# Kernel optimization log

Hardware: AMD Instinct MI355X
Metric: run time of the kernel (lower is better)

Reference implementation:

```python
import jax, jax.numpy as jnp
import numpy as np

N = 65536        # total nodes
E = 2097152      # total edges (avg degree 32)
B = 1024         # graphs / proteins
FXD = 78         # atom feature dim
DIM = 32         # GIN hidden dim
EMB = 128        # protein embedding dim
OUTD = 128       # output_dim
VOCAB = 26       # CHARPROTLEN + 1
PLEN = 1000      # protein sequence length (conv in_channels)
KS = 8           # conv kernel size
CLEN = EMB - KS + 1  # 121
NF = 32          # n_filters


def setup_inputs() -> dict:
    key = jax.random.key(0)
    ks = jax.random.split(key, 30)
    g = lambda k, s: (jax.random.normal(k, s, dtype=jnp.float32) * 0.05)
    inp = {
        "x": jax.random.normal(ks[0], (N, FXD), dtype=jnp.float32),
        "edge_index": jax.random.randint(ks[1], (2, E), 0, N, dtype=jnp.int32),
        "batch": jnp.sort(jax.random.randint(ks[2], (N,), 0, B, dtype=jnp.int32)),
        "target": jax.random.randint(ks[3], (B, PLEN), 0, VOCAB, dtype=jnp.int32),
        # GIN layer 1 MLP
        "w1a": g(ks[4], (FXD, DIM)), "b1a": jnp.zeros((DIM,), jnp.float32),
        "w1b": g(ks[5], (DIM, DIM)), "b1b": jnp.zeros((DIM,), jnp.float32),
        # GIN layers 2-5 MLPs (stacked)
        "wa": g(ks[6], (4, DIM, DIM)), "ba": jnp.zeros((4, DIM), jnp.float32),
        "wb": g(ks[7], (4, DIM, DIM)), "bb": jnp.zeros((4, DIM), jnp.float32),
        # BatchNorm affine params for bn1..bn5
        "gamma": jnp.ones((5, DIM), jnp.float32),
        "beta": jnp.zeros((5, DIM), jnp.float32),
        # drug head
        "w_fcxd": g(ks[8], (DIM, OUTD)), "b_fcxd": jnp.zeros((OUTD,), jnp.float32),
        # protein branch
        "emb": g(ks[9], (VOCAB, EMB)),
        "conv_w": g(ks[10], (NF, PLEN, KS)),  # OIH layout
        "conv_b": jnp.zeros((NF,), jnp.float32),
        "w_fcxt": g(ks[11], (NF * CLEN, OUTD)), "b_fcxt": jnp.zeros((OUTD,), jnp.float32),
        # joint head
        "w_fc1": g(ks[12], (256, 1024)), "b_fc1": jnp.zeros((1024,), jnp.float32),
        "w_fc2": g(ks[13], (1024, 256)), "b_fc2": jnp.zeros((256,), jnp.float32),
        "w_out": g(ks[14], (256, 1)), "b_out": jnp.zeros((1,), jnp.float32),
    }
    return inp


def reference(x, edge_index, batch, target,
              w1a, b1a, w1b, b1b, wa, ba, wb, bb, gamma, beta,
              w_fcxd, b_fcxd, emb, conv_w, conv_b, w_fcxt, b_fcxt,
              w_fc1, b_fc1, w_fc2, b_fc2, w_out, b_out):
    n_nodes = x.shape[0]
    n_graphs = target.shape[0]
    src, dst = edge_index[0], edge_index[1]

    def gin_bn(h, wi, bi, wo, bo, g, bt):
        # GINConv (eps=0): nn((1+eps)*x + sum_{j->i} x_j), then ReLU, then BatchNorm1d (batch stats)
        agg = jax.ops.segment_sum(h[src], dst, num_segments=n_nodes) + h
        h = jnp.maximum(agg @ wi + bi, 0.0) @ wo + bo
        h = jnp.maximum(h, 0.0)
        m = h.mean(axis=0)
        v = h.var(axis=0)  # biased, matches torch BN normalization
        return g * (h - m) * jax.lax.rsqrt(v + 1e-5) + bt

    h = gin_bn(x, w1a, b1a, w1b, b1b, gamma[0], beta[0])
    for i in range(4):
        h = gin_bn(h, wa[i], ba[i], wb[i], bb[i], gamma[i + 1], beta[i + 1])

    # global add pool over graphs
    hg = jax.ops.segment_sum(h, batch, num_segments=n_graphs)  # [B, 32]
    xd = jnp.maximum(hg @ w_fcxd + b_fcxd, 0.0)  # [B, 128] (dropout inactive in eval)

    # protein branch: embed then Conv1d over the embedding axis (in_channels = seq positions)
    e = emb[target]  # [B, 1000, 128]
    c = jax.lax.conv_general_dilated(e, conv_w, window_strides=(1,), padding="VALID",
                                     dimension_numbers=("NCH", "OIH", "NCH"))
    c = c + conv_b[None, :, None]  # [B, 32, 121]
    xt = c.reshape(n_graphs, NF * CLEN) @ w_fcxt + b_fcxt  # [B, 128], no activation in original

    xc = jnp.concatenate([xd, xt], axis=1)  # [B, 256]
    xc = jnp.maximum(xc @ w_fc1 + b_fc1, 0.0)
    xc = jnp.maximum(xc @ w_fc2 + b_fc2, 0.0)
    return xc @ w_out + b_out  # [B, 1]
```

## Files before the change

### kernel.cpp

```cpp
#include <hip/hip_runtime.h>
#include <hip/hip_fp16.h>

#define N_NODES 65536
#define N_EDGES 2097152
#define NB      1024
#define FXD     78
#define DIM     32
#define EMBD    128
#define OUTD    128
#define VOCAB   26
#define PLEN    1000
#define KS      8
#define CLEN    121
#define NF      32
#define FCX     (NF*CLEN)
#define NBKT    256
#define EPB     8192
#define NSLICE  256


__global__ __launch_bounds__(256) void k_bhist(
    const int* __restrict__ ei, int* __restrict__ bktCnt)
{
    __shared__ int h[NBKT];
    int tid = threadIdx.x;
    h[tid] = 0;
    __syncthreads();
    long base = (long)blockIdx.x * EPB;
    #pragma unroll 4
    for (int q=0; q<EPB/256; ++q) {
        int d = ei[N_EDGES + base + q*256 + tid];
        atomicAdd(&h[d>>8], 1);
    }
    __syncthreads();
    atomicAdd(&bktCnt[tid], h[tid]);
}

__global__ __launch_bounds__(256) void k_bscan(
    const int* __restrict__ bktCnt, int* __restrict__ bktBase, int* __restrict__ bktCur)
{
    __shared__ int s[NBKT];
    int t = threadIdx.x;
    int v = bktCnt[t];
    s[t] = v;
    __syncthreads();
    for (int off=1; off<256; off<<=1) {
        int tv = (t >= off) ? s[t-off] : 0;
        __syncthreads();
        s[t] += tv;
        __syncthreads();
    }
    int ex = s[t] - v;
    bktBase[t] = ex;
    bktCur[t] = ex;
    if (t == 255) bktBase[256] = s[255];
}

__global__ __launch_bounds__(256) void k_bucketA(
    const int* __restrict__ ei, int* __restrict__ bktCur, unsigned int* __restrict__ pairs)
{
    __shared__ unsigned int raw[EPB];
    __shared__ unsigned int srt[EPB];
    __shared__ unsigned char bOf[EPB];
    __shared__ int hist[NBKT], sc[NBKT], lcur[NBKT], gbase[NBKT];
    int tid = threadIdx.x;
    hist[tid] = 0;
    __syncthreads();
    int eb = blockIdx.x * EPB;
    for (int i=tid; i<EPB; i+=256) {
        int s = ei[eb+i];
        int d = ei[N_EDGES+eb+i];
        raw[i] = ((unsigned int)d<<16) | (unsigned int)s;
        atomicAdd(&hist[d>>8], 1);
    }
    __syncthreads();
    int v = hist[tid];
    sc[tid] = v;
    __syncthreads();
    for (int off=1; off<256; off<<=1) {
        int tv = (tid >= off) ? sc[tid-off] : 0;
        __syncthreads();
        sc[tid] += tv;
        __syncthreads();
    }
    int ex = sc[tid] - v;
    sc[tid] = ex;
    lcur[tid] = ex;
    gbase[tid] = atomicAdd(&bktCur[tid], v);
    __syncthreads();
    for (int i=tid; i<EPB; i+=256) {
        unsigned int p = raw[i];
        int k = p >> 24;
        int pos = atomicAdd(&lcur[k], 1);
        srt[pos] = p;
        bOf[pos] = (unsigned char)k;
    }
    __syncthreads();
    for (int i=tid; i<EPB; i+=256) {
        int k = bOf[i];
        pairs[gbase[k] + (i - sc[k])] = srt[i];
    }
}

__global__ __launch_bounds__(256) void k_fillB(
    const int* __restrict__ bktBase, const unsigned int* __restrict__ pairs,
    int* __restrict__ rowptr, int* __restrict__ csr)
{
    __shared__ int hist[256], sc[256], cur[256];
    int b = blockIdx.x, tid = threadIdx.x;
    int node0 = b*256;
    hist[tid] = 0;
    __syncthreads();
    int s = bktBase[b], e = bktBase[b+1];
    for (int i = s + tid; i < e; i += 256)
        atomicAdd(&hist[(pairs[i] >> 16) & 255], 1);
    __syncthreads();
    int v = hist[tid];
    sc[tid] = v;
    __syncthreads();
    for (int off=1; off<256; off<<=1) {
        int tv = (tid >= off) ? sc[tid-off] : 0;
        __syncthreads();
        sc[tid] += tv;
        __syncthreads();
    }
    int base = s + sc[tid] - v;
    rowptr[node0 + tid] = base;
    cur[tid] = base;
    if (b == NBKT-1 && tid == 255) rowptr[N_NODES] = N_EDGES;
    __syncthreads();
    for (int i = s + tid; i < e; i += 256) {
        unsigned int p = pairs[i];
        int pos = atomicAdd(&cur[(p >> 16) & 255], 1);
        csr[pos] = (int)(p & 0xFFFFu);
    }
}


__global__ __launch_bounds__(256) void k_l1_transform(
    const float* __restrict__ x, const float* __restrict__ w,
    __half* __restrict__ t)
{
    __shared__ float wS[FXD*DIM];
    for (int i = threadIdx.x; i < FXD*DIM; i += 256) wS[i] = w[i];
    __syncthreads();
    int node = blockIdx.x*256 + threadIdx.x;
    float acc[DIM];
    #pragma unroll
    for (int d=0; d<DIM; ++d) acc[d] = 0.f;
    const float* xr = x + (long)node*FXD;
    for (int j=0; j<FXD; ++j) {
        float xv = xr[j];
        #pragma unroll
        for (int d=0; d<DIM; ++d) acc[d] += xv * wS[j*DIM+d];
    }
    union { __half2 h2[16]; uint4 u4[4]; } pk;
    #pragma unroll
    for (int q=0; q<16; ++q) pk.h2[q] = __floats2half2_rn(acc[2*q], acc[2*q+1]);
    uint4* dst4 = (uint4*)(t + (long)node*DIM);
    #pragma unroll
    for (int q=0; q<4; ++q) dst4[q] = pk.u4[q];
}

__global__ __launch_bounds__(256) void k_transform(
    const float* __restrict__ z, const float* __restrict__ part,
    const float* __restrict__ gamma, const float* __restrict__ beta, int layer,
    const float* __restrict__ w, __half* __restrict__ t)
{
    __shared__ float wS[DIM*DIM];
    __shared__ float red[4][64];
    __shared__ float sS[2*DIM];
    int tid = threadIdx.x;
    for (int i=tid; i<DIM*DIM; i+=256) wS[i] = w[i];
    {
        int ch = tid & 63, qq = tid >> 6;
        float s = 0.f;
        for (int i = qq*64; i < qq*64 + 64; ++i) s += part[(i<<6) + ch];
        red[qq][ch] = s;
    }
    __syncthreads();
    if (tid < DIM) {
        float tots = red[0][tid]+red[1][tid]+red[2][tid]+red[3][tid];
        float totq = red[0][DIM+tid]+red[1][DIM+tid]+red[2][DIM+tid]+red[3][DIM+tid];
        float mean = tots * (1.f/N_NODES);
        float var  = totq * (1.f/N_NODES) - mean*mean;
        float sc = gamma[layer*DIM+tid] * rsqrtf(var + 1e-5f);
        sS[tid] = sc;
        sS[DIM+tid] = beta[layer*DIM+tid] - mean*sc;
    }
    __syncthreads();
    int node = blockIdx.x*256 + tid;
    float h[DIM];
    const float4* z4 = (const float4*)(z + (long)node*DIM);
    #pragma unroll
    for (int q=0; q<DIM/4; ++q) {
        float4 v = z4[q];
        h[q*4+0]=v.x; h[q*4+1]=v.y; h[q*4+2]=v.z; h[q*4+3]=v.w;
    }
    #pragma unroll
    for (int d=0; d<DIM; ++d) h[d] = h[d]*sS[d] + sS[DIM+d];
    float acc[DIM];
    #pragma unroll
    for (int d=0; d<DIM; ++d) acc[d] = 0.f;
    #pragma unroll
    for (int j=0; j<DIM; ++j) {
        float hv = h[j];
        #pragma unroll
        for (int d=0; d<DIM; ++d) acc[d] += hv * wS[j*DIM+d];
    }
    union { __half2 h2[16]; uint4 u4[4]; } pk;
    #pragma unroll
    for (int q=0; q<16; ++q) pk.h2[q] = __floats2half2_rn(acc[2*q], acc[2*q+1]);
    uint4* dst4 = (uint4*)(t + (long)node*DIM);
    #pragma unroll
    for (int q=0; q<4; ++q) dst4[q] = pk.u4[q];
}

__global__ __launch_bounds__(256) void k_gather_mlp(
    const int* __restrict__ rowptr, const int* __restrict__ csr,
    const __half* __restrict__ t,
    const float* __restrict__ bi, const float* __restrict__ wo, const float* __restrict__ bo,
    float* __restrict__ z, float* __restrict__ part)
{
    __shared__ float wS[DIM*DIM];
    __shared__ float bS[2*DIM];
    __shared__ float stS[2*DIM];
    int tid = threadIdx.x;
    for (int i=tid; i<DIM*DIM; i+=256) wS[i]=wo[i];
    if (tid<DIM) bS[tid]=bi[tid];
    else if (tid<2*DIM) bS[tid]=bo[tid-DIM];
    if (tid<2*DIM) stS[tid]=0.f;
    __syncthreads();
    int g = tid >> 3;
    int l = tid & 7;
    int node = blockIdx.x*32 + g;
    const uint2* t4 = (const uint2*)t;
    uint2 sv = t4[(long)node*8 + l];
    float2 p0 = __half22float2(*(const __half2*)&sv.x);
    float2 p1 = __half22float2(*(const __half2*)&sv.y);
    float a0=p0.x, a1=p0.y, a2=p1.x, a3=p1.y;
    float c0=0.f, c1=0.f, c2=0.f, c3=0.f;
    int s0 = rowptr[node], s1 = rowptr[node+1];
    int e = s0;
    for (; e+8 <= s1; e+=8) {
        int myIdx = csr[e + l];
        #pragma unroll
        for (int k=0; k<8; ++k) {
            int idx = __shfl(myIdx, k, 8);
            uint2 v = t4[(long)idx*8 + l];
            float2 q0 = __half22float2(*(const __half2*)&v.x);
            float2 q1 = __half22float2(*(const __half2*)&v.y);
            if (k & 1) { c0+=q0.x; c1+=q0.y; c2+=q1.x; c3+=q1.y; }
            else       { a0+=q0.x; a1+=q0.y; a2+=q1.x; a3+=q1.y; }
        }
    }
    if (e+4 <= s1) {
        int myIdx = csr[e + (l & 3)];
        #pragma unroll
        for (int k=0; k<4; ++k) {
            int idx = __shfl(myIdx, k, 8);
            uint2 v = t4[(long)idx*8 + l];
            float2 q0 = __half22float2(*(const __half2*)&v.x);
            float2 q1 = __half22float2(*(const __half2*)&v.y);
            if (k & 1) { c0+=q0.x; c1+=q0.y; c2+=q1.x; c3+=q1.y; }
            else       { a0+=q0.x; a1+=q0.y; a2+=q1.x; a3+=q1.y; }
        }
        e += 4;
    }
    for (; e<s1; ++e) {
        uint2 v = t4[(long)csr[e]*8 + l];
        float2 q0 = __half22float2(*(const __half2*)&v.x);
        float2 q1 = __half22float2(*(const __half2*)&v.y);
        a0+=q0.x; a1+=q0.y; a2+=q1.x; a3+=q1.y;
    }
    float ua[4];
    ua[0] = fmaxf(a0+c0 + bS[4*l+0], 0.f);
    ua[1] = fmaxf(a1+c1 + bS[4*l+1], 0.f);
    ua[2] = fmaxf(a2+c2 + bS[4*l+2], 0.f);
    ua[3] = fmaxf(a3+c3 + bS[4*l+3], 0.f);
    float zz[4];
    #pragma unroll
    for (int q=0; q<4; ++q) zz[q] = bS[DIM + 4*l + q];
    const float4* w4 = (const float4*)wS;
    #pragma unroll
    for (int j=0; j<DIM; ++j) {
        float uj = __shfl(ua[j & 3], j >> 2, 8);
        float4 wv = w4[j*8 + l];
        zz[0]+=uj*wv.x; zz[1]+=uj*wv.y; zz[2]+=uj*wv.z; zz[3]+=uj*wv.w;
    }
    #pragma unroll
    for (int q=0; q<4; ++q) zz[q] = fmaxf(zz[q], 0.f);
    ((float4*)z)[(long)node*8 + l] = make_float4(zz[0], zz[1], zz[2], zz[3]);
    float sr[4], qr[4];
    #pragma unroll
    for (int q=0; q<4; ++q) { sr[q] = zz[q]; qr[q] = zz[q]*zz[q]; }
    #pragma unroll
    for (int q=0; q<4; ++q) {
        sr[q] += __shfl_down(sr[q], 32, 64); qr[q] += __shfl_down(qr[q], 32, 64);
        sr[q] += __shfl_down(sr[q], 16, 64); qr[q] += __shfl_down(qr[q], 16, 64);
        sr[q] += __shfl_down(sr[q],  8, 64); qr[q] += __shfl_down(qr[q],  8, 64);
    }
    if ((tid & 63) < 8) {
        #pragma unroll
        for (int q=0; q<4; ++q) {
            atomicAdd(&stS[4*l+q],       sr[q]);
            atomicAdd(&stS[DIM+4*l+q],   qr[q]);
        }
    }
    __syncthreads();
    if (tid < 2*DIM)
        atomicAdd(&part[((blockIdx.x & (NSLICE-1))<<6) + tid], stS[tid]);
}

__global__ __launch_bounds__(256) void k_scaleshift(
    const float* __restrict__ part,
    const float* __restrict__ gamma, const float* __restrict__ beta,
    int layer, float* __restrict__ ss)
{
    __shared__ float red[4][64];
    __shared__ float totS[64];
    int t = threadIdx.x;
    int ch = t & 63, q = t >> 6;
    float s = 0.f;
    for (int i = q*64; i < q*64 + 64; ++i) s += part[(i<<6) + ch];
    red[q][ch] = s;
    __syncthreads();
    if (t < 64) totS[t] = red[0][t]+red[1][t]+red[2][t]+red[3][t];
    __syncthreads();
    if (t < DIM) {
        float mean = totS[t] * (1.f/N_NODES);
        float var  = totS[DIM+t] * (1.f/N_NODES) - mean*mean;
        float sc = gamma[layer*DIM+t] * rsqrtf(var + 1e-5f);
        ss[t] = sc;
        ss[DIM+t] = beta[layer*DIM+t] - mean*sc;
    }
}

__global__ __launch_bounds__(256) void k_pool(
    const float* __restrict__ z, const float* __restrict__ ss,
    const int* __restrict__ batch, float* __restrict__ hg)
{
    int tid = threadIdx.x;
    int node = blockIdx.x*32 + (tid>>3);
    int cq = tid & 7;
    float4 v = ((const float4*)z)[(long)node*8 + cq];
    float4 sc = ((const float4*)ss)[cq];
    float4 sh = ((const float4*)ss)[8 + cq];
    v.x = v.x*sc.x + sh.x; v.y = v.y*sc.y + sh.y;
    v.z = v.z*sc.z + sh.z; v.w = v.w*sc.w + sh.w;
    int b = batch[node];
    int b0 = __shfl(b, 0, 64);
    int b7 = __shfl(b, 63, 64);
    if (b0 == b7) {
        #pragma unroll
        for (int off=8; off<64; off<<=1) {
            v.x += __shfl_xor(v.x, off, 64);
            v.y += __shfl_xor(v.y, off, 64);
            v.z += __shfl_xor(v.z, off, 64);
            v.w += __shfl_xor(v.w, off, 64);
        }
        if ((tid & 63) < 8) {
            float* dst = hg + (long)b0*DIM + cq*4;
            atomicAdd(dst+0, v.x); atomicAdd(dst+1, v.y);
            atomicAdd(dst+2, v.z); atomicAdd(dst+3, v.w);
        }
    } else {
        float* dst = hg + (long)b*DIM + cq*4;
        atomicAdd(dst+0, v.x); atomicAdd(dst+1, v.y);
        atomicAdd(dst+2, v.z); atomicAdd(dst+3, v.w);
    }
}

__global__ __launch_bounds__(128) void k_xd(
    const float* __restrict__ hg, const float* __restrict__ w,
    const float* __restrict__ bias, float* __restrict__ xc)
{
    int b = blockIdx.x, n = threadIdx.x;
    __shared__ float hS[DIM];
    if (n < DIM) hS[n] = hg[b*DIM+n];
    __syncthreads();
    float acc = bias[n];
    #pragma unroll
    for (int r=0; r<DIM; ++r) acc += hS[r]*w[r*OUTD+n];
    xc[b*256 + n] = fmaxf(acc, 0.f);
}


__global__ __launch_bounds__(256) void k_cw_transpose(
    const float* __restrict__ cw, __half* __restrict__ cwT)
{
    int g = blockIdx.x*256 + threadIdx.x;
    int i = g >> 8;
    int j = g & 255;
    int o = j >> 3, k = j & 7;
    cwT[g] = __float2half(cw[o*(PLEN*KS) + i*KS + k]);
}

__global__ __launch_bounds__(256) void k_convA(
    const int* __restrict__ target, const __half* __restrict__ cwTh,
    __half* __restrict__ G)
{
    __shared__ int sortedS[PLEN];
    __shared__ int meta[3*VOCAB+2];
    int* cntS = meta;
    int* segS = meta + VOCAB;
    int* curS = meta + 2*VOCAB + 1;
    int bb = blockIdx.x, j = threadIdx.x;
    int b = bb >> 1, sub = bb & 1;
    if (j < VOCAB) cntS[j] = 0;
    __syncthreads();
    int tloc[4];
    #pragma unroll
    for (int q=0; q<4; ++q) {
        int i = j + q*256;
        if (i < PLEN) {
            tloc[q] = target[b*PLEN+i];
            atomicAdd(&cntS[tloc[q]], 1);
        } else tloc[q] = -1;
    }
    __syncthreads();
    if (j == 0) {
        int run = 0;
        for (int v=0; v<VOCAB; ++v) { segS[v]=run; run += cntS[v]; }
        segS[VOCAB] = run;
    }
    __syncthreads();
    if (j < VOCAB) curS[j] = segS[j];
    __syncthreads();
    #pragma unroll
    for (int q=0; q<4; ++q) {
        int i = j + q*256;
        if (i < PLEN) {
            int pos = atomicAdd(&curS[tloc[q]], 1);
            sortedS[pos] = i;
        }
    }
    __syncthreads();
    int w = j >> 6;
    int lane = j & 63;
    int half32 = lane >> 5;
    int c32 = lane & 31;
    const uint4* cw4 = (const uint4*)cwTh;
    __half2 hz = __float2half2_rn(0.f);
    int v0 = 13*sub, v1 = v0 + 13;
    int segbase = segS[v0];
    int tot = segS[v1] - segbase;
    for (int v=v0; v<v1; ++v) {
        int s = segS[v], e2 = segS[v+1];
        int wv = (tot > 0) ? ((s - segbase)*4)/tot : 0;
        if (wv > 3) wv = 3;
        if (wv != w) continue;
        float facc[8];
        #pragma unroll
        for (int q=0; q<8; ++q) facc[q] = 0.f;
        int p = s;
        for (; p+16 <= e2; p += 16) {
            __half2 h0=hz, h1=hz, h2=hz, h3=hz;
            #pragma unroll
            for (int u=0; u<8; ++u) {
                int i0 = sortedS[p+2*u], i1 = sortedS[p+2*u+1];
                int row = half32 ? i1 : i0;
                uint4 q4 = cw4[row*32 + c32];
                const __half2* hh = (const __half2*)&q4;
                h0 = __hadd2(h0, hh[0]); h1 = __hadd2(h1, hh[1]);
                h2 = __hadd2(h2, hh[2]); h3 = __hadd2(h3, hh[3]);
            }
            float2 f0=__half22float2(h0), f1=__half22float2(h1),
                   f2=__half22float2(h2), f3=__half22float2(h3);
            facc[0]+=f0.x; facc[1]+=f0.y; facc[2]+=f1.x; facc[3]+=f1.y;
            facc[4]+=f2.x; facc[5]+=f2.y; facc[6]+=f3.x; facc[7]+=f3.y;
        }
        for (; p+2 <= e2; p += 2) {
            int i0 = sortedS[p], i1 = sortedS[p+1];
            int row = half32 ? i1 : i0;
            uint4 q4 = cw4[row*32 + c32];
            const __half2* hh = (const __half2*)&q4;
            float2 f0=__half22float2(hh[0]), f1=__half22float2(hh[1]),
                   f2=__half22float2(hh[2]), f3=__half22float2(hh[3]);
            facc[0]+=f0.x; facc[1]+=f0.y; facc[2]+=f1.x; facc[3]+=f1.y;
            facc[4]+=f2.x; facc[5]+=f2.y; facc[6]+=f3.x; facc[7]+=f3.y;
        }
        if (p < e2 && half32 == 0) {
            uint4 q4 = cw4[sortedS[p]*32 + c32];
            const __half2* hh = (const __half2*)&q4;
            float2 f0=__half22float2(hh[0]), f1=__half22float2(hh[1]),
                   f2=__half22float2(hh[2]), f3=__half22float2(hh[3]);
            facc[0]+=f0.x; facc[1]+=f0.y; facc[2]+=f1.x; facc[3]+=f1.y;
            facc[4]+=f2.x; facc[5]+=f2.y; facc[6]+=f3.x; facc[7]+=f3.y;
        }
        #pragma unroll
        for (int q=0; q<8; ++q) facc[q] += __shfl_xor(facc[q], 32, 64);
        if (half32 == 0) {
            __half2 o0 = __floats2half2_rn(facc[0], facc[1]);
            __half2 o1 = __floats2half2_rn(facc[2], facc[3]);
            __half2 o2 = __floats2half2_rn(facc[4], facc[5]);
            __half2 o3 = __floats2half2_rn(facc[6], facc[7]);
            uint4 pk;
            pk.x = *(unsigned int*)&o0; pk.y = *(unsigned int*)&o1;
            pk.z = *(unsigned int*)&o2; pk.w = *(unsigned int*)&o3;
            ((uint4*)(G + ((long)b*VOCAB + v)*256))[c32] = pk;
        }
    }
}

__global__ __launch_bounds__(256) void k_mprep(
    const float* __restrict__ emb, const float* __restrict__ w,
    const float* __restrict__ conv_b, float* __restrict__ M,
    float* __restrict__ C0)
{
    __shared__ float eS[EMBD];
    int v = blockIdx.x >> 5, o = blockIdx.x & 31;
    int tid = threadIdx.x;
    if (tid < EMBD) eS[tid] = emb[v*EMBD + tid];
    __syncthreads();
    int n = tid & 127, kb = tid >> 7;
    float acc[4] = {0.f, 0.f, 0.f, 0.f};
    float c0 = 0.f;
    const float* wp = w + (long)(o*CLEN)*OUTD + n;
    for (int t2=0; t2<CLEN; ++t2) {
        float wv = wp[(long)t2*OUTD];
        c0 += wv;
        #pragma unroll
        for (int q=0; q<4; ++q) acc[q] += eS[t2 + kb + 2*q] * wv;
    }
    long base = ((long)(v*256 + o*8)) * 128 + n;
    #pragma unroll
    for (int q=0; q<4; ++q) M[base + (long)(kb + 2*q)*128] = acc[q];
    if (v == 0 && kb == 0) atomicAdd(&C0[n], c0 * conv_b[o]);
}

#define XG_GB  16
#define XG_NS  16
#define XG_K   (VOCAB*256)
#define XG_KS  (XG_K/XG_NS)
#define XG_BK  32
#define XG_NCH (XG_KS/XG_BK)
__global__ __launch_bounds__(256) void k_xtg(
    const __half* __restrict__ G, const float* __restrict__ M,
    float* __restrict__ xtp)
{
    __shared__ float bS[XG_BK][128];
    __shared__ __half aS[XG_GB][XG_BK];
    int b0 = blockIdx.x * XG_GB;
    int ks0 = blockIdx.y * XG_KS;
    int tid = threadIdx.x;
    int g2 = tid >> 5, co = tid & 31;
    int ag = tid >> 4, au = tid & 15;
    const unsigned int* G32 = (const unsigned int*)G;
    float breg[16];
    unsigned int areg;
    {
        int k0 = ks0;
        #pragma unroll
        for (int q=0; q<16; ++q) {
            int idx = tid + q*256;
            breg[q] = M[(long)(k0 + (idx>>7))*128 + (idx & 127)];
        }
        areg = G32[(long)(b0+ag)*3328 + (k0>>1) + au];
    }
    float acc[2][4];
    #pragma unroll
    for (int q=0; q<2; ++q)
      #pragma unroll
      for (int p=0; p<4; ++p) acc[q][p] = 0.f;
    for (int ch=0; ch<XG_NCH; ++ch) {
        #pragma unroll
        for (int q=0; q<16; ++q) {
            int idx = tid + q*256;
            bS[idx>>7][idx & 127] = breg[q];
        }
        ((unsigned int*)aS)[ag*16 + au] = areg;
        __syncthreads();
        if (ch+1 < XG_NCH) {
            int k0 = ks0 + (ch+1)*XG_BK;
            #pragma unroll
            for (int q=0; q<16; ++q) {
                int idx = tid + q*256;
                breg[q] = M[(long)(k0 + (idx>>7))*128 + (idx & 127)];
            }
            areg = G32[(long)(b0+ag)*3328 + (k0>>1) + au];
        }
        #pragma unroll
        for (int kk=0; kk<XG_BK; ++kk) {
            float a0 = __half2float(aS[2*g2  ][kk]);
            float a1 = __half2float(aS[2*g2+1][kk]);
            float4 wv = *(const float4*)&bS[kk][co*4];
            acc[0][0]+=a0*wv.x; acc[0][1]+=a0*wv.y;
            acc[0][2]+=a0*wv.z; acc[0][3]+=a0*wv.w;
            acc[1][0]+=a1*wv.x; acc[1][1]+=a1*wv.y;
            acc[1][2]+=a1*wv.z; acc[1][3]+=a1*wv.w;
        }
        __syncthreads();
    }
    #pragma unroll
    for (int q=0; q<2; ++q) {
        int g = b0 + 2*g2 + q;
        float4* dst = (float4*)(xtp + ((long)blockIdx.y*NB + g)*128);
        dst[co] = make_float4(acc[q][0], acc[q][1], acc[q][2], acc[q][3]);
    }
}

__global__ __launch_bounds__(256) void k_xtg_red(
    const float* __restrict__ xtp, const float* __restrict__ bias,
    const float* __restrict__ C0, float* __restrict__ xc)
{
    int p = blockIdx.x*256 + threadIdx.x;
    int g = p >> 5, c4 = p & 31;
    const float4* src = (const float4*)xtp;
    float4 s = src[(long)g*32 + c4];
    #pragma unroll
    for (int y=1; y<XG_NS; ++y) {
        float4 v = src[((long)y*NB + g)*32 + c4];
        s.x += v.x; s.y += v.y; s.z += v.z; s.w += v.w;
    }
    float4 bv = ((const float4*)bias)[c4];
    float4 cv = ((const float4*)C0)[c4];
    s.x += bv.x + cv.x; s.y += bv.y + cv.y;
    s.z += bv.z + cv.z; s.w += bv.w + cv.w;
    ((float4*)(xc + g*256 + 128))[c4] = s;
}


#define FC1_NS 4
#define FC1_KR 64
__global__ __launch_bounds__(256) void k_fc1(
    const float* __restrict__ xc, const float* __restrict__ w,
    float* __restrict__ y1p)
{
    __shared__ float xS[4][FC1_KR];
    int b0 = blockIdx.x*4;
    int r0 = blockIdx.y*FC1_KR;
    int n = threadIdx.x;
    xS[n>>6][n&63] = xc[(b0 + (n>>6))*256 + r0 + (n&63)];
    __syncthreads();
    float acc[4][4];
    #pragma unroll
    for (int q=0;q<4;++q)
      #pragma unroll
      for (int m=0;m<4;++m) acc[q][m]=0.f;
    for (int r=0; r<FC1_KR; ++r) {
        float x0=xS[0][r], x1=xS[1][r], x2=xS[2][r], x3=xS[3][r];
        #pragma unroll
        for (int m=0; m<4; ++m) {
            float wv = w[(long)(r0+r)*1024 + m*256 + n];
            acc[0][m]+=x0*wv; acc[1][m]+=x1*wv;
            acc[2][m]+=x2*wv; acc[3][m]+=x3*wv;
        }
    }
    long base = ((long)blockIdx.y*NB + b0)*1024;
    #pragma unroll
    for (int q=0; q<4; ++q)
        #pragma unroll
        for (int m=0; m<4; ++m)
            y1p[base + (long)q*1024 + m*256 + n] = acc[q][m];
}

__global__ __launch_bounds__(256) void k_fc1_red(
    const float* __restrict__ y1p, const float* __restrict__ bias,
    float* __restrict__ y)
{
    int p = blockIdx.x*256 + threadIdx.x;
    int g = p >> 8, c4 = p & 255;
    const float4* src = (const float4*)y1p;
    float4 s = src[(long)g*256 + c4];
    #pragma unroll
    for (int yq=1; yq<FC1_NS; ++yq) {
        float4 v = src[((long)yq*NB + g)*256 + c4];
        s.x+=v.x; s.y+=v.y; s.z+=v.z; s.w+=v.w;
    }
    float4 bv = ((const float4*)bias)[c4];
    s.x = fmaxf(s.x+bv.x, 0.f); s.y = fmaxf(s.y+bv.y, 0.f);
    s.z = fmaxf(s.z+bv.z, 0.f); s.w = fmaxf(s.w+bv.w, 0.f);
    ((float4*)y)[(long)g*256 + c4] = s;
}

#define FC2_NS 8
#define FC2_KR 128
__global__ __launch_bounds__(256) void k_fc2(
    const float* __restrict__ y, const float* __restrict__ w,
    float* __restrict__ y2p)
{
    __shared__ float xS[4][FC2_KR];
    int b0 = blockIdx.x*4;
    int r0 = blockIdx.y*FC2_KR;
    int n = threadIdx.x;
    {
        int e1 = n + 256;
        xS[n>>7][n&127]   = y[(b0 + (n>>7))*1024  + r0 + (n&127)];
        xS[e1>>7][e1&127] = y[(b0 + (e1>>7))*1024 + r0 + (e1&127)];
    }
    __syncthreads();
    float acc[4] = {0.f, 0.f, 0.f, 0.f};
    for (int r=0; r<FC2_KR; ++r) {
        float wv = w[(long)(r0+r)*256 + n];
        acc[0]+=xS[0][r]*wv; acc[1]+=xS[1][r]*wv;
        acc[2]+=xS[2][r]*wv; acc[3]+=xS[3][r]*wv;
    }
    long base = ((long)blockIdx.y*NB + b0)*256;
    #pragma unroll
    for (int q=0; q<4; ++q) y2p[base + q*256 + n] = acc[q];
}

__global__ __launch_bounds__(256) void k_fc2_red(
    const float* __restrict__ y2p, const float* __restrict__ bias,
    float* __restrict__ y2)
{
    int p = blockIdx.x*256 + threadIdx.x;
    int g = p >> 6, c4 = p & 63;
    const float4* src = (const float4*)y2p;
    float4 s = src[(long)g*64 + c4];
    #pragma unroll
    for (int yq=1; yq<FC2_NS; ++yq) {
        float4 v = src[((long)yq*NB + g)*64 + c4];
        s.x+=v.x; s.y+=v.y; s.z+=v.z; s.w+=v.w;
    }
    float4 bv = ((const float4*)bias)[c4];
    s.x = fmaxf(s.x+bv.x, 0.f); s.y = fmaxf(s.y+bv.y, 0.f);
    s.z = fmaxf(s.z+bv.z, 0.f); s.w = fmaxf(s.w+bv.w, 0.f);
    ((float4*)y2)[(long)g*64 + c4] = s;
}

__global__ __launch_bounds__(256) void k_out(
    const float* __restrict__ y2, const float* __restrict__ w,
    const float* __restrict__ bias, float* __restrict__ out)
{
    int b = blockIdx.x, n = threadIdx.x;
    float v = y2[b*256 + n] * w[n];
    #pragma unroll
    for (int off=32; off; off>>=1) v += __shfl_down(v, off, 64);
    __shared__ float red[4];
    if ((n & 63) == 0) red[n >> 6] = v;
    __syncthreads();
    if (n == 0) out[b] = red[0]+red[1]+red[2]+red[3] + bias[0];
}


extern "C" void kernel_launch(void* const* d_in, const int* in_sizes, int n_in,
                              void* d_out, int out_size, void* d_ws, size_t ws_size,
                              hipStream_t stream) {
    const float* x      = (const float*)d_in[0];
    const int*   ei     = (const int*)  d_in[1];
    const int*   batch  = (const int*)  d_in[2];
    const int*   target = (const int*)  d_in[3];
    const float* w1a    = (const float*)d_in[4];
    const float* b1a    = (const float*)d_in[5];
    const float* w1b    = (const float*)d_in[6];
    const float* b1b    = (const float*)d_in[7];
    const float* wa     = (const float*)d_in[8];
    const float* ba     = (const float*)d_in[9];
    const float* wb     = (const float*)d_in[10];
    const float* bb     = (const float*)d_in[11];
    const float* gamma  = (const float*)d_in[12];
    const float* beta   = (const float*)d_in[13];
    const float* w_fcxd = (const float*)d_in[14];
    const float* b_fcxd = (const float*)d_in[15];
    const float* emb    = (const float*)d_in[16];
    const float* conv_w = (const float*)d_in[17];
    const float* conv_b = (const float*)d_in[18];
    const float* w_fcxt = (const float*)d_in[19];
    const float* b_fcxt = (const float*)d_in[20];
    const float* w_fc1  = (const float*)d_in[21];
    const float* b_fc1  = (const float*)d_in[22];
    const float* w_fc2  = (const float*)d_in[23];
    const float* b_fc2  = (const float*)d_in[24];
    const float* w_out  = (const float*)d_in[25];
    const float* b_out  = (const float*)d_in[26];

    float* ws      = (float*)d_ws;
    __half* tH     = (__half*)ws;
    float* z       = ws + 1048576;
    unsigned int* pairs = (unsigned int*)(z + (size_t)N_NODES*DIM);
    int*   csr     = (int*)(pairs + N_EDGES);
    int*   rowptr  = csr + N_EDGES;
    int*   bktCnt  = rowptr + (N_NODES + 8);
    int*   bktBase = bktCnt + 256;
    int*   bktCur  = bktBase + 264;
    float* ss      = (float*)(bktCur + 256);
    float* hg      = ss + 64;
    float* cwT     = hg + (size_t)NB*DIM;
    float* cbuf    = cwT + 256000;
    float* xc      = cbuf + (size_t)NB*FCX;
    float* y1      = xc + (size_t)NB*256;
    float* y2      = y1 + (size_t)NB*1024;
    float* part    = y2 + (size_t)NB*256;
    __half* cwTh   = (__half*)cwT;
    __half* Gbuf   = (__half*)z;
    float* Mbuf    = cbuf;
    float* C0buf   = cbuf + 851968;
    float* xtp     = cbuf + 860160;
    float* y1p     = ws;
    float* y2p     = ws + 4194304;

    hipMemsetAsync(bktCnt, 0, 256*sizeof(int), stream);
    k_bhist<<<NBKT, 256, 0, stream>>>(ei, bktCnt);
    k_bscan<<<1, 256, 0, stream>>>(bktCnt, bktBase, bktCur);
    k_bucketA<<<NBKT, 256, 0, stream>>>(ei, bktCur, pairs);
    k_fillB<<<NBKT, 256, 0, stream>>>(bktBase, pairs, rowptr, csr);

    hipMemsetAsync(C0buf, 0, 128*sizeof(float), stream);
    k_cw_transpose<<<1000, 256, 0, stream>>>(conv_w, cwTh);
    k_mprep<<<VOCAB*32, 256, 0, stream>>>(emb, w_fcxt, conv_b, Mbuf, C0buf);
    k_convA<<<2*NB, 256, 0, stream>>>(target, cwTh, Gbuf);
    k_xtg<<<dim3(NB/XG_GB, XG_NS), 256, 0, stream>>>(Gbuf, Mbuf, xtp);
    k_xtg_red<<<(NB*DIM)/256, 256, 0, stream>>>(xtp, b_fcxt, C0buf, xc);

    hipMemsetAsync(part, 0, 5*NSLICE*64*sizeof(float), stream);
    for (int l=0; l<5; ++l) {
        if (l == 0)
            k_l1_transform<<<N_NODES/256, 256, 0, stream>>>(x, w1a, tH);
        else
            k_transform<<<N_NODES/256, 256, 0, stream>>>(
                z, part + (size_t)(l-1)*NSLICE*64, gamma, beta, l-1,
                wa + (size_t)(l-1)*DIM*DIM, tH);
        const float* bi = (l==0) ? b1a : ba + (size_t)(l-1)*DIM;
        const float* wo = (l==0) ? w1b : wb + (size_t)(l-1)*DIM*DIM;
        const float* bo = (l==0) ? b1b : bb + (size_t)(l-1)*DIM;
        k_gather_mlp<<<N_NODES/32, 256, 0, stream>>>(
            rowptr, csr, tH, bi, wo, bo, z, part + (size_t)l*NSLICE*64);
    }
    k_scaleshift<<<1, 256, 0, stream>>>(part + (size_t)4*NSLICE*64, gamma, beta, 4, ss);

    hipMemsetAsync(hg, 0, (size_t)NB*DIM*sizeof(float), stream);
    k_pool<<<N_NODES/32, 256, 0, stream>>>(z, ss, batch, hg);
    k_xd<<<NB, 128, 0, stream>>>(hg, w_fcxd, b_fcxd, xc);

    k_fc1<<<dim3(NB/4, FC1_NS), 256, 0, stream>>>(xc, w_fc1, y1p);
    k_fc1_red<<<1024, 256, 0, stream>>>(y1p, b_fc1, y1);
    k_fc2<<<dim3(NB/4, FC2_NS), 256, 0, stream>>>(y1, w_fc2, y2p);
    k_fc2_red<<<256, 256, 0, stream>>>(y2p, b_fc2, y2);
    k_out<<<NB, 256, 0, stream>>>(y2, w_out, b_out, (float*)d_out);
}
```

Before: 625.8 us.

## Restructure k_xtg GEMM with split-K across warps and register-held A tiles

Reworks the k_xtg tiled GEMM so that each thread holds 8 graph rows of fp16 A data in registers, loaded directly from global memory as uint4. The k-slice is split across four 64-thread groups, and the partial sums are combined with a shared-memory tree reduction at the end. B tile loads and stores are widened to float4, the A shared buffer is removed, and launch bounds request 4 blocks per CU. The aim is more FMAs per shared-memory load and fewer scalar memory ops. The cost is higher register pressure and extra reduction synchronisation.

```diff
diff --git a/kernel.cpp b/kernel.cpp
--- a/kernel.cpp
+++ b/kernel.cpp
@@ -535,68 +535,103 @@
 #define XG_KS  (XG_K/XG_NS)
 #define XG_BK  32
 #define XG_NCH (XG_KS/XG_BK)
-__global__ __launch_bounds__(256) void k_xtg(
+__global__ __launch_bounds__(256, 4) void k_xtg(
     const __half* __restrict__ G, const float* __restrict__ M,
     float* __restrict__ xtp)
 {
     __shared__ float bS[XG_BK][128];
-    __shared__ __half aS[XG_GB][XG_BK];
     int b0 = blockIdx.x * XG_GB;
     int ks0 = blockIdx.y * XG_KS;
     int tid = threadIdx.x;
-    int g2 = tid >> 5, co = tid & 31;
-    int ag = tid >> 4, au = tid & 15;
-    const unsigned int* G32 = (const unsigned int*)G;
-    float breg[16];
-    unsigned int areg;
+    int th  = tid >> 6;
+    int grp = (tid >> 5) & 1;
+    int co  = tid & 31;
+    const uint4*  G4 = (const uint4*)G;
+    const float4* M4 = (const float4*)M;
+    float4 breg[4];
     {
         int k0 = ks0;
         #pragma unroll
-        for (int q=0; q<16; ++q) {
-            int idx = tid + q*256;
-            breg[q] = M[(long)(k0 + (idx>>7))*128 + (idx & 127)];
-        }
-        areg = G32[(long)(b0+ag)*3328 + (k0>>1) + au];
-    }
-    float acc[2][4];
-    #pragma unroll
-    for (int q=0; q<2; ++q)
-      #pragma unroll
-      for (int p=0; p<4; ++p) acc[q][p] = 0.f;
+        for (int q=0; q<4; ++q) {
+            int i4 = tid + q*256;
+            breg[q] = M4[(long)(k0 + (i4>>5))*32 + (i4 & 31)];
+        }
+    }
+    float4 acc[8];
+    #pragma unroll
+    for (int q=0; q<8; ++q) acc[q] = make_float4(0.f, 0.f, 0.f, 0.f);
+    long arowbase = (long)(b0 + grp*8) * 832;
     for (int ch=0; ch<XG_NCH; ++ch) {
-        #pragma unroll
-        for (int q=0; q<16; ++q) {
-            int idx = tid + q*256;
-            bS[idx>>7][idx & 127] = breg[q];
-        }
-        ((unsigned int*)aS)[ag*16 + au] = areg;
+        int k0 = ks0 + ch*XG_BK;
+        #pragma unroll
+        for (int q=0; q<4; ++q) {
+            int i4 = tid + q*256;
+            *(float4*)&bS[i4>>5][(i4 & 31)*4] = breg[q];
+        }
+        uint4 Ar[8];
+        {
+            long kq = (k0 >> 3) + th;
+            #pragma unroll
+            for (int q=0; q<8; ++q) Ar[q] = G4[arowbase + (long)q*832 + kq];
+        }
         __syncthreads();
         if (ch+1 < XG_NCH) {
-            int k0 = ks0 + (ch+1)*XG_BK;
+            int k1 = k0 + XG_BK;
             #pragma unroll
-            for (int q=0; q<16; ++q) {
-                int idx = tid + q*256;
-                breg[q] = M[(long)(k0 + (idx>>7))*128 + (idx & 127)];
+            for (int q=0; q<4; ++q) {
+                int i4 = tid + q*256;
+                breg[q] = M4[(long)(k1 + (i4>>5))*32 + (i4 & 31)];
             }
-            areg = G32[(long)(b0+ag)*3328 + (k0>>1) + au];
-        }
-        #pragma unroll
-        for (int kk=0; kk<XG_BK; ++kk) {
-            float a0 = __half2float(aS[2*g2  ][kk]);
-            float a1 = __half2float(aS[2*g2+1][kk]);
-            float4 wv = *(const float4*)&bS[kk][co*4];
-            acc[0][0]+=a0*wv.x; acc[0][1]+=a0*wv.y;
-            acc[0][2]+=a0*wv.z; acc[0][3]+=a0*wv.w;
-            acc[1][0]+=a1*wv.x; acc[1][1]+=a1*wv.y;
-            acc[1][2]+=a1*wv.z; acc[1][3]+=a1*wv.w;
+        }
+        #pragma unroll
+        for (int h=0; h<4; ++h) {
+            int kk = th*8 + h*2;
+            float4 bv0 = *(const float4*)&bS[kk  ][co*4];
+            float4 bv1 = *(const float4*)&bS[kk+1][co*4];
+            #pragma unroll
+            for (int q=0; q<8; ++q) {
+                __half2 hv = ((const __half2*)&Ar[q])[h];
+                float2 f = __half22float2(hv);
+                acc[q].x += f.x*bv0.x + f.y*bv1.x;
+                acc[q].y += f.x*bv0.y + f.y*bv1.y;
+                acc[q].z += f.x*bv0.z + f.y*bv1.z;
+                acc[q].w += f.x*bv0.w + f.y*bv1.w;
+            }
         }
         __syncthreads();
     }
-    #pragma unroll
-    for (int q=0; q<2; ++q) {
-        int g = b0 + 2*g2 + q;
-        float4* dst = (float4*)(xtp + ((long)blockIdx.y*NB + g)*128);
-        dst[co] = make_float4(acc[q][0], acc[q][1], acc[q][2], acc[q][3]);
+    float* red = (float*)bS;
+    if (th >= 2) {
+        int slot = tid - 128;
+        #pragma unroll
+        for (int q=0; q<8; ++q) *(float4*)&red[slot*32 + q*4] = acc[q];
+    }
+    __syncthreads();
+    if (th < 2) {
+        int slot = tid;
+        #pragma unroll
+        for (int q=0; q<8; ++q) {
+            float4 v = *(const float4*)&red[slot*32 + q*4];
+            acc[q].x+=v.x; acc[q].y+=v.y; acc[q].z+=v.z; acc[q].w+=v.w;
+        }
+    }
+    __syncthreads();
+    if (th == 1) {
+        int slot = tid - 64;
+        #pragma unroll
+        for (int q=0; q<8; ++q) *(float4*)&red[slot*32 + q*4] = acc[q];
+    }
+    __syncthreads();
+    if (th == 0) {
+        int slot = tid;
+        #pragma unroll
+        for (int q=0; q<8; ++q) {
+            float4 v = *(const float4*)&red[slot*32 + q*4];
+            float4 o = make_float4(acc[q].x+v.x, acc[q].y+v.y,
+                                   acc[q].z+v.z, acc[q].w+v.w);
+            int g = b0 + grp*8 + q;
+            ((float4*)(xtp + ((long)blockIdx.y*NB + g)*128))[co] = o;
+        }
     }
 }
 
```

Result: slower. 834.2 us (+33.3%).
